# Performance work log

Measured on AMD Instinct MI355X. Metric: run time of the kernel, lower is better.

## Reference

```python
import jax, jax.numpy as jnp
import numpy as np

EPS = 1e-5

def _layer_norm(x, w, b):
    mu = jnp.mean(x, axis=-1, keepdims=True)
    var = jnp.mean((x - mu) ** 2, axis=-1, keepdims=True)
    return (x - mu) * jax.lax.rsqrt(var + EPS) * w + b

def setup_inputs() -> dict:
    H = 2048
    B, T = 4, 2048
    key = jax.random.key(0)
    ks = jax.random.split(key, 12)
    s = 0.02
    return {
        "hidden_state": jax.random.normal(ks[0], (B, T, H), dtype=jnp.float32),
        "ln_w": jnp.ones((H,), jnp.float32),
        "ln_b": jnp.zeros((H,), jnp.float32),
        "Wk": jax.random.normal(ks[1], (H, H), jnp.float32) * s,
        "Wv": jax.random.normal(ks[2], (H, H), jnp.float32) * s,
        "Wr": jax.random.normal(ks[3], (H, H), jnp.float32) * s,
        "Wo": jax.random.normal(ks[4], (H, H), jnp.float32) * s,
        "mix_k": jax.random.uniform(ks[5], (H,), jnp.float32),
        "mix_v": jax.random.uniform(ks[6], (H,), jnp.float32),
        "mix_r": jax.random.uniform(ks[7], (H,), jnp.float32),
        "time_decay": jax.random.normal(ks[8], (H,), jnp.float32) * 0.5,
        "current_token_weight": jax.random.normal(ks[9], (H,), jnp.float32) * 0.5,
    }

def _wkv(k, v, time_decay, curr_w):
    # k, v: [B, T, H]; max-stabilized RWKV recurrence, scanned over time.
    B, T, H = k.shape
    decay = -jnp.exp(time_decay)  # [H]
    num0 = jnp.zeros((B, H), k.dtype)
    den0 = jnp.zeros((B, H), k.dtype)
    norm0 = jnp.full((B, H), -jnp.inf, k.dtype)

    def step(carry, kv):
        num, den, norm = carry
        kt, vt = kv  # [B, H]
        ct = curr_w + kt
        cn = jnp.maximum(ct, norm)
        e_prev = jnp.exp(norm - cn)
        e_cur = jnp.exp(ct - cn)
        out = (e_prev * num + e_cur * vt) / (e_prev * den + e_cur)
        dpn = decay + norm
        new_norm = jnp.maximum(dpn, kt)
        e_d = jnp.exp(dpn - new_norm)
        e_k = jnp.exp(kt - new_norm)
        return (e_d * num + e_k * vt, e_d * den + e_k, new_norm), out

    kT = jnp.swapaxes(k, 0, 1)  # [T, B, H]
    vT = jnp.swapaxes(v, 0, 1)
    (num, den, norm), outs = jax.lax.scan(step, (num0, den0, norm0), (kT, vT))
    return jnp.swapaxes(outs, 0, 1), num, den, norm

def reference(hidden_state, ln_w, ln_b, Wk, Wv, Wr, Wo, mix_k, mix_v, mix_r,
              time_decay, current_token_weight):
    residual = hidden_state
    x = _layer_norm(hidden_state, ln_w, ln_b)  # [B, T, H]
    B, T, H = x.shape
    # shifted input: previous token (zeros for t=0 since previous_state is None)
    sx = jnp.concatenate([jnp.zeros((B, 1, H), x.dtype), x[:, :-1, :]], axis=1)
    xk = sx + mix_k * (x - sx)
    xv = sx + mix_v * (x - sx)
    xr = sx + mix_r * (x - sx)
    r = jax.nn.sigmoid(jnp.einsum('bth,oh->bto', xr, Wr))
    k = jnp.einsum('bth,oh->bto', xk, Wk)
    v = jnp.einsum('bth,oh->bto', xv, Wv)
    wkv, num, den, norm = _wkv(k, v, time_decay, current_token_weight)
    rwkv = jnp.einsum('bth,oh->bto', r * wkv, Wo)
    out = residual + rwkv
    return (out, (x[:, -1, :], num, den, norm))
```

## Files before the change

kernel.cpp:

```cpp
#include <hip/hip_runtime.h>
#include <hip/hip_bf16.h>
#include <stdint.h>

#define B_ 4
#define T_ 2048
#define H_ 2048
#define BT_ (B_ * T_)
#define BH_ (B_ * H_)
#define CH_ 32
#define CL_ (T_ / CH_)
#define NKT_ (H_ / 64)

typedef __bf16 bf16x8 __attribute__((ext_vector_type(8)));
typedef float f32x4 __attribute__((ext_vector_type(4)));

__device__ inline void async16(const void* g, void* l) {
  __builtin_amdgcn_global_load_lds(
      (__attribute__((address_space(1))) uint32_t*)(void*)(uintptr_t)g,
      (__attribute__((address_space(3))) uint32_t*)l,
      16, 0, 0);
}

__global__ __launch_bounds__(256) void cvt_bf16_kernel(
    const float* __restrict__ w0, const float* __restrict__ w1,
    const float* __restrict__ w2, const float* __restrict__ w3,
    __bf16* __restrict__ dst ) {
  const float* srcs[4] = {w0, w1, w2, w3};
  const float* src = srcs[blockIdx.y];
  __bf16* d = dst + (size_t)blockIdx.y * H_ * H_;
  int i = (blockIdx.x * 256 + threadIdx.x) * 8;
  const float4* s4 = (const float4*)(src + i);
  float4 a = s4[0], b = s4[1];
  bf16x8 o;
  o[0] = (__bf16)a.x; o[1] = (__bf16)a.y; o[2] = (__bf16)a.z; o[3] = (__bf16)a.w;
  o[4] = (__bf16)b.x; o[5] = (__bf16)b.y; o[6] = (__bf16)b.z; o[7] = (__bf16)b.w;
  *(bf16x8*)(d + i) = o;
}

__global__ __launch_bounds__(256) void ln_mix_kernel(
    const float* __restrict__ h, const float* __restrict__ lnw,
    const float* __restrict__ lnb, const float* __restrict__ mk,
    const float* __restrict__ mv, const float* __restrict__ mr,
    __bf16* __restrict__ xk, __bf16* __restrict__ xv, __bf16* __restrict__ xr,
    float* __restrict__ xlast) {
  const int row = blockIdx.x;
  const int t = row & (T_ - 1);
  const int tid = threadIdx.x;
  const bool hasprev = (t != 0);

  const float4* cr = (const float4*)(h + (size_t)row * H_);
  float4 c0 = cr[tid * 2 + 0], c1 = cr[tid * 2 + 1];
  float4 p0 = {0.f, 0.f, 0.f, 0.f}, p1 = {0.f, 0.f, 0.f, 0.f};
  if (hasprev) {
    const float4* pr = (const float4*)(h + (size_t)(row - 1) * H_);
    p0 = pr[tid * 2 + 0]; p1 = pr[tid * 2 + 1];
  }
  float4 red;
  red.x = c0.x + c0.y + c0.z + c0.w + c1.x + c1.y + c1.z + c1.w;
  red.y = c0.x * c0.x + c0.y * c0.y + c0.z * c0.z + c0.w * c0.w +
          c1.x * c1.x + c1.y * c1.y + c1.z * c1.z + c1.w * c1.w;
  red.z = p0.x + p0.y + p0.z + p0.w + p1.x + p1.y + p1.z + p1.w;
  red.w = p0.x * p0.x + p0.y * p0.y + p0.z * p0.z + p0.w * p0.w +
          p1.x * p1.x + p1.y * p1.y + p1.z * p1.z + p1.w * p1.w;
  #pragma unroll
  for (int off = 32; off; off >>= 1) {
    red.x += __shfl_down(red.x, off);
    red.y += __shfl_down(red.y, off);
    red.z += __shfl_down(red.z, off);
    red.w += __shfl_down(red.w, off);
  }
  __shared__ float4 rbuf_[4];
  const int lane = tid & 63, wid = tid >> 6;
  if (lane == 0) rbuf_[wid] = red;
  __syncthreads();
  float4 tot;
  tot.x = rbuf_[0].x + rbuf_[1].x + rbuf_[2].x + rbuf_[3].x;
  tot.y = rbuf_[0].y + rbuf_[1].y + rbuf_[2].y + rbuf_[3].y;
  tot.z = rbuf_[0].z + rbuf_[1].z + rbuf_[2].z + rbuf_[3].z;
  tot.w = rbuf_[0].w + rbuf_[1].w + rbuf_[2].w + rbuf_[3].w;

  const float inv = 1.0f / (float)H_;
  float mu = tot.x * inv;
  float rstd = rsqrtf(fmaxf(tot.y * inv - mu * mu, 0.f) + 1e-5f);
  float mup = tot.z * inv;
  float rstdp = rsqrtf(fmaxf(tot.w * inv - mup * mup, 0.f) + 1e-5f);

  float xc[8] = {c0.x, c0.y, c0.z, c0.w, c1.x, c1.y, c1.z, c1.w};
  float xp[8] = {p0.x, p0.y, p0.z, p0.w, p1.x, p1.y, p1.z, p1.w};
  const float4* W4 = (const float4*)lnw;
  const float4* Bv4 = (const float4*)lnb;
  const float4* MK4 = (const float4*)mk;
  const float4* MV4 = (const float4*)mv;
  const float4* MR4 = (const float4*)mr;
  float4 w0 = W4[tid * 2], w1 = W4[tid * 2 + 1];
  float4 b0 = Bv4[tid * 2], b1 = Bv4[tid * 2 + 1];
  float4 k0 = MK4[tid * 2], k1 = MK4[tid * 2 + 1];
  float4 v0 = MV4[tid * 2], v1 = MV4[tid * 2 + 1];
  float4 r0 = MR4[tid * 2], r1 = MR4[tid * 2 + 1];
  float wa[8] = {w0.x, w0.y, w0.z, w0.w, w1.x, w1.y, w1.z, w1.w};
  float ba[8] = {b0.x, b0.y, b0.z, b0.w, b1.x, b1.y, b1.z, b1.w};
  float ka[8] = {k0.x, k0.y, k0.z, k0.w, k1.x, k1.y, k1.z, k1.w};
  float va[8] = {v0.x, v0.y, v0.z, v0.w, v1.x, v1.y, v1.z, v1.w};
  float ra[8] = {r0.x, r0.y, r0.z, r0.w, r1.x, r1.y, r1.z, r1.w};

  bf16x8 ok_, ov_, or_;
  float xls[8];
  #pragma unroll
  for (int e = 0; e < 8; e++) {
    float x = (xc[e] - mu) * rstd * wa[e] + ba[e];
    float sx = hasprev ? (xp[e] - mup) * rstdp * wa[e] + ba[e] : 0.f;
    ok_[e] = (__bf16)(sx + ka[e] * (x - sx));
    ov_[e] = (__bf16)(sx + va[e] * (x - sx));
    or_[e] = (__bf16)(sx + ra[e] * (x - sx));
    xls[e] = x;
  }
  size_t obase = (size_t)row * H_ + tid * 8;
  *(bf16x8*)(xk + obase) = ok_;
  *(bf16x8*)(xv + obase) = ov_;
  *(bf16x8*)(xr + obase) = or_;
  if (t == T_ - 1) {
    float* dst = xlast + (size_t)(row >> 11) * H_ + tid * 8;
    #pragma unroll
    for (int e = 0; e < 8; e++) dst[e] = xls[e];
  }
}

template <int WO>
__global__ __launch_bounds__(256, 2) void gemm128(
    const __bf16* __restrict__ A0, const __bf16* __restrict__ A1,
    const __bf16* __restrict__ A2, const __bf16* __restrict__ Wb,
    __bf16* __restrict__ o0, __bf16* __restrict__ o1, __bf16* __restrict__ o2,
    float* __restrict__ outf, const float* __restrict__ resid) {
  __shared__ __align__(16) char ring[2][32768];

  const int NB = WO ? 1024 : 3072;
  const int wgid = blockIdx.x;
  const int lin = (wgid & 7) * (NB / 8) + (wgid >> 3);
  int z, l;
  if (WO) { z = 0; l = lin; }
  else    { z = lin >> 10; l = lin & 1023; }
  const int bm = l >> 4;
  const int bn = l & 15;

  const __bf16* A = (WO || z == 0) ? A0 : (z == 1 ? A1 : A2);
  const __bf16* Bw = Wb + (size_t)z * H_ * H_;
  __bf16* ob = (z == 0) ? o0 : (z == 1 ? o1 : o2);

  const int tid = threadIdx.x;
  const int lane = tid & 63, wv = tid >> 6;
  const int wm = wv >> 1;
  const int wn = wv & 1;
  const int rr = lane & 15, q = lane >> 4;

  f32x4 acc[4][4];
  #pragma unroll
  for (int m = 0; m < 4; m++)
    #pragma unroll
    for (int n = 0; n < 4; n++) acc[m][n] = (f32x4){0.f, 0.f, 0.f, 0.f};

  const char* Ag = (const char*)A + (size_t)(bm * 128) * (H_ * 2);
  const char* Bg = (const char*)Bw + (size_t)(bn * 128) * (H_ * 2);

  const int srow = wv * 8 + (lane >> 3);
  const int scol = ((lane & 7) ^ (lane >> 3)) << 4;
  const int rsw = rr & 7;

#define STAGE_TILE(kt_, buf_)                                                   \
  {                                                                             \
    char* base_ = ring[buf_];                                                   \
    _Pragma("unroll")                                                           \
    for (int mh_ = 0; mh_ < 2; mh_++) {                                         \
      const char* Mg_ = mh_ ? Bg : Ag;                                          \
      _Pragma("unroll")                                                         \
      for (int rd_ = 0; rd_ < 4; rd_++) {                                       \
        char* dst_ = base_ + mh_ * 16384 + rd_ * 4096 + wv * 1024;              \
        const char* src_ = Mg_ + (size_t)(rd_ * 32 + srow) * (H_ * 2)           \
                           + (kt_) * 128 + scol;                                \
        async16(src_, dst_);                                                    \
      }                                                                         \
    }                                                                           \
  }

  STAGE_TILE(0, 0);
  asm volatile("s_waitcnt vmcnt(0)" ::: "memory");
  __builtin_amdgcn_s_barrier();

  for (int kt = 0; kt < NKT_; kt++) {
    const int cur = kt & 1, nxt = cur ^ 1;
    const char* Alds = ring[cur];
    const char* Blds = ring[cur] + 16384;

    if (kt + 1 < NKT_) STAGE_TILE(kt + 1, nxt);

    bf16x8 bfr[4][2];
    #pragma unroll
    for (int ni = 0; ni < 4; ni++)
      #pragma unroll
      for (int ks = 0; ks < 2; ks++) {
        int row_t = wn * 64 + ni * 16 + rr;
        bfr[ni][ks] = *(const bf16x8*)(Blds + row_t * 128 +
                                       (((ks * 4 + q) ^ rsw) << 4));
      }

    #pragma unroll
    for (int mi = 0; mi < 4; mi++) {
      bf16x8 af[2];
      #pragma unroll
      for (int ks = 0; ks < 2; ks++) {
        int row_t = wm * 64 + mi * 16 + rr;
        af[ks] = *(const bf16x8*)(Alds + row_t * 128 +
                                  (((ks * 4 + q) ^ rsw) << 4));
      }
      #pragma unroll
      for (int ks = 0; ks < 2; ks++)
        #pragma unroll
        for (int ni = 0; ni < 4; ni++)
          acc[mi][ni] = __builtin_amdgcn_mfma_f32_16x16x32_bf16(
              af[ks], bfr[ni][ks], acc[mi][ni], 0, 0, 0);
    }

    if (kt + 1 < NKT_) {
      asm volatile("s_waitcnt vmcnt(0)" ::: "memory");
      __builtin_amdgcn_s_barrier();
    }
  }
#undef STAGE_TILE

  const int r0 = bm * 128 + wm * 64 + q * 4;
  const int c0 = bn * 128 + wn * 64 + rr;
  #pragma unroll
  for (int mi = 0; mi < 4; mi++) {
    #pragma unroll
    for (int ni = 0; ni < 4; ni++) {
      int col = c0 + ni * 16;
      #pragma unroll
      for (int rg = 0; rg < 4; rg++) {
        int rowg = r0 + mi * 16 + rg;
        size_t idx = (size_t)rowg * H_ + col;
        float vv = acc[mi][ni][rg];
        if (WO) {
          outf[idx] = resid[idx] + vv;
        } else if (z == 2) {
          ob[idx] = (__bf16)(1.f / (1.f + __expf(-vv)));
        } else {
          ob[idx] = (__bf16)vv;
        }
      }
    }
  }
}

__global__ __launch_bounds__(256) void wkv_pass1(
    const __bf16* __restrict__ k, const __bf16* __restrict__ v,
    const float* __restrict__ td,
    float* __restrict__ cs_num, float* __restrict__ cs_den,
    float* __restrict__ cs_norm) {
  const int id = blockIdx.x * 256 + threadIdx.x;
  const int c = blockIdx.y;
  const int b = id >> 11;
  const int hh = id & (H_ - 1);
  const float decay = -__expf(td[hh]);
  float num = 0.f, den = 0.f, norm = -INFINITY;

  const int UN = 16;
  for (int t0 = c * CL_; t0 < (c + 1) * CL_; t0 += UN) {
    float kk[UN], vv[UN];
    size_t base = ((size_t)b * T_ + t0) * H_ + hh;
    #pragma unroll
    for (int i = 0; i < UN; i++) {
      kk[i] = (float)k[base + (size_t)i * H_];
      vv[i] = (float)v[base + (size_t)i * H_];
    }
    #pragma unroll
    for (int i = 0; i < UN; i++) {
      float dpn = decay + norm;
      float nn = fmaxf(dpn, kk[i]);
      float ed = __expf(dpn - nn), ek = __expf(kk[i] - nn);
      num = ed * num + ek * vv[i];
      den = ed * den + ek;
      norm = nn;
    }
  }
  cs_num[c * BH_ + id] = num;
  cs_den[c * BH_ + id] = den;
  cs_norm[c * BH_ + id] = norm;
}

__global__ __launch_bounds__(256) void wkv_scan(
    const float* __restrict__ cs_num, const float* __restrict__ cs_den,
    const float* __restrict__ cs_norm, const float* __restrict__ td,
    float* __restrict__ px_num, float* __restrict__ px_den,
    float* __restrict__ px_norm) {
  const int id = blockIdx.x * 256 + threadIdx.x;
  const int hh = id & (H_ - 1);
  const float Lw = -__expf(td[hh]) * (float)CL_;
  float num = 0.f, den = 0.f, norm = -INFINITY;
  for (int c = 0; c < CH_; c++) {
    px_num[c * BH_ + id] = num;
    px_den[c * BH_ + id] = den;
    px_norm[c * BH_ + id] = norm;
    float n_c = cs_num[c * BH_ + id];
    float d_c = cs_den[c * BH_ + id];
    float m_c = cs_norm[c * BH_ + id];
    float sn = norm + Lw;
    float on = fmaxf(sn, m_c);
    float ea = __expf(sn - on), eb = __expf(m_c - on);
    num = ea * num + eb * n_c;
    den = ea * den + eb * d_c;
    norm = on;
  }
}

__global__ __launch_bounds__(256) void wkv_pass2(
    const __bf16* __restrict__ k, const __bf16* __restrict__ v,
    const __bf16* __restrict__ r, const float* __restrict__ td,
    const float* __restrict__ cw,
    const float* __restrict__ px_num, const float* __restrict__ px_den,
    const float* __restrict__ px_norm,
    __bf16* __restrict__ a, float* __restrict__ ndn) {
  const int id = blockIdx.x * 256 + threadIdx.x;
  const int c = blockIdx.y;
  const int b = id >> 11;
  const int hh = id & (H_ - 1);
  const float decay = -__expf(td[hh]);
  const float cwv = cw[hh];
  float num = px_num[c * BH_ + id];
  float den = px_den[c * BH_ + id];
  float norm = px_norm[c * BH_ + id];

  const int UN = 16;
  for (int t0 = c * CL_; t0 < (c + 1) * CL_; t0 += UN) {
    float kk[UN], vv[UN], rrv[UN];
    size_t base = ((size_t)b * T_ + t0) * H_ + hh;
    #pragma unroll
    for (int i = 0; i < UN; i++) {
      kk[i] = (float)k[base + (size_t)i * H_];
      vv[i] = (float)v[base + (size_t)i * H_];
      rrv[i] = (float)r[base + (size_t)i * H_];
    }
    #pragma unroll
    for (int i = 0; i < UN; i++) {
      float kt = kk[i], vt = vv[i];
      float ct = cwv + kt;
      float cn = fmaxf(ct, norm);
      float ep = __expf(norm - cn), ec = __expf(ct - cn);
      float o = (ep * num + ec * vt) / (ep * den + ec);
      a[base + (size_t)i * H_] = (__bf16)(rrv[i] * o);
      float dpn = decay + norm;
      float nn = fmaxf(dpn, kt);
      float ed = __expf(dpn - nn), ek = __expf(kt - nn);
      num = ed * num + ek * vt;
      den = ed * den + ek;
      norm = nn;
    }
  }
  if (c == CH_ - 1) {
    ndn[id] = num;
    ndn[BH_ + id] = den;
    ndn[2 * BH_ + id] = norm;
  }
}

extern "C" void kernel_launch(void* const* d_in, const int* in_sizes, int n_in,
                              void* d_out, int out_size, void* d_ws, size_t ws_size,
                              hipStream_t stream) {
  const float* h   = (const float*)d_in[0];
  const float* lnw = (const float*)d_in[1];
  const float* lnb = (const float*)d_in[2];
  const float* Wk  = (const float*)d_in[3];
  const float* Wv  = (const float*)d_in[4];
  const float* Wr  = (const float*)d_in[5];
  const float* Wo  = (const float*)d_in[6];
  const float* mk  = (const float*)d_in[7];
  const float* mv  = (const float*)d_in[8];
  const float* mr  = (const float*)d_in[9];
  const float* td  = (const float*)d_in[10];
  const float* cw  = (const float*)d_in[11];

  char* ws = (char*)d_ws;
  const size_t MB = 1048576;
  __bf16* xk   = (__bf16*)(ws);
  __bf16* xv   = (__bf16*)(ws + 32 * MB);
  __bf16* xr   = (__bf16*)(ws + 64 * MB);
  __bf16* kbuf = (__bf16*)(ws + 96 * MB);
  __bf16* vbuf = (__bf16*)(ws + 128 * MB);
  __bf16* W16  = (__bf16*)(ws + 160 * MB);
  __bf16* rbuf = (__bf16*)(ws + 192 * MB);
  __bf16* Wo16 = W16 + 3 * (size_t)H_ * H_;
  float* cs_num  = (float*)(ws + 64 * MB);
  float* cs_den  = cs_num + (size_t)CH_ * BH_;
  float* cs_norm = cs_den + (size_t)CH_ * BH_;
  float* px_num  = cs_norm + (size_t)CH_ * BH_;
  float* px_den  = px_num + (size_t)CH_ * BH_;
  float* px_norm = px_den + (size_t)CH_ * BH_;

  float* out  = (float*)d_out;
  float* xlast = out + (size_t)BT_ * H_;
  float* ndn   = xlast + (size_t)B_ * H_;

  dim3 cg((H_ * H_) / (256 * 8), 4);
  cvt_bf16_kernel<<<cg, 256, 0, stream>>>(Wk, Wv, Wr, Wo, W16);

  ln_mix_kernel<<<BT_, 256, 0, stream>>>(h, lnw, lnb, mk, mv, mr, xk, xv, xr, xlast);

  gemm128<0><<<3072, 256, 0, stream>>>(xk, xv, xr, W16, kbuf, vbuf, rbuf,
                                       nullptr, nullptr);

  dim3 wg(BH_ / 256, CH_);
  wkv_pass1<<<wg, 256, 0, stream>>>(kbuf, vbuf, td, cs_num, cs_den, cs_norm);
  wkv_scan<<<BH_ / 256, 256, 0, stream>>>(cs_num, cs_den, cs_norm, td,
                                          px_num, px_den, px_norm);
  wkv_pass2<<<wg, 256, 0, stream>>>(kbuf, vbuf, rbuf, td, cw,
                                    px_num, px_den, px_norm,
                                    xk , ndn);

  gemm128<1><<<1024, 256, 0, stream>>>(xk, nullptr, nullptr, Wo16,
                                       nullptr, nullptr, nullptr, out, h);
}
```

Before: 400.5 us.

## Split GEMM into dedicated KVR and Wo kernels with larger Wo tiles

Replaces the templated GEMM with two kernels. The fused K/V/R GEMM gets a new block-index swizzle that groups 8 M-tiles per N column for L2 reuse. The output projection becomes a 256x256-tile, 512-thread kernel with 128KB of double-buffered LDS, which raises arithmetic intensity per loaded tile. The trade-off is lower occupancy (one block per CU) and only 256 blocks for that GEMM, which may underfill the device.

```diff
diff --git a/kernel.cpp b/kernel.cpp
--- a/kernel.cpp
+++ b/kernel.cpp
@@ -125,24 +125,21 @@
   }
 }
 
-template <int WO>
-__global__ __launch_bounds__(256, 2) void gemm128(
+__global__ __launch_bounds__(256, 2) void gemm_kvr(
     const __bf16* __restrict__ A0, const __bf16* __restrict__ A1,
     const __bf16* __restrict__ A2, const __bf16* __restrict__ Wb,
-    __bf16* __restrict__ o0, __bf16* __restrict__ o1, __bf16* __restrict__ o2,
-    float* __restrict__ outf, const float* __restrict__ resid) {
+    __bf16* __restrict__ o0, __bf16* __restrict__ o1, __bf16* __restrict__ o2) {
   __shared__ __align__(16) char ring[2][32768];
 
-  const int NB = WO ? 1024 : 3072;
   const int wgid = blockIdx.x;
-  const int lin = (wgid & 7) * (NB / 8) + (wgid >> 3);
-  int z, l;
-  if (WO) { z = 0; l = lin; }
-  else    { z = lin >> 10; l = lin & 1023; }
-  const int bm = l >> 4;
-  const int bn = l & 15;
-
-  const __bf16* A = (WO || z == 0) ? A0 : (z == 1 ? A1 : A2);
+  const int z = wgid >> 10;
+  const int g = wgid & 1023;
+  const int x = g & 7;
+  const int i = g >> 3;
+  const int bm = x * 8 + (i & 7);
+  const int bn = i >> 3;
+
+  const __bf16* A = (z == 0) ? A0 : (z == 1 ? A1 : A2);
   const __bf16* Bw = Wb + (size_t)z * H_ * H_;
   __bf16* ob = (z == 0) ? o0 : (z == 1 ? o1 : o2);
 
@@ -238,13 +235,125 @@
         int rowg = r0 + mi * 16 + rg;
         size_t idx = (size_t)rowg * H_ + col;
         float vv = acc[mi][ni][rg];
-        if (WO) {
-          outf[idx] = resid[idx] + vv;
-        } else if (z == 2) {
+        if (z == 2) {
           ob[idx] = (__bf16)(1.f / (1.f + __expf(-vv)));
         } else {
           ob[idx] = (__bf16)vv;
         }
+      }
+    }
+  }
+}
+
+__global__ __launch_bounds__(512, 1) void gemm_wo(
+    const __bf16* __restrict__ A, const __bf16* __restrict__ Bw,
+    float* __restrict__ outf, const float* __restrict__ resid) {
+  __shared__ __align__(16) char ring[2][65536];
+
+  const int wgid = blockIdx.x;
+  const int lin = (wgid & 7) * 32 + (wgid >> 3);
+  const int bm = lin >> 3;
+  const int bn = lin & 7;
+
+  const int tid = threadIdx.x;
+  const int lane = tid & 63, wv = tid >> 6;
+  const int wm = wv >> 2;
+  const int wn = wv & 3;
+  const int rr = lane & 15, q = lane >> 4;
+
+  f32x4 acc[8][4];
+  #pragma unroll
+  for (int m = 0; m < 8; m++)
+    #pragma unroll
+    for (int n = 0; n < 4; n++) acc[m][n] = (f32x4){0.f, 0.f, 0.f, 0.f};
+
+  const char* Ag = (const char*)A + (size_t)(bm * 256) * (H_ * 2);
+  const char* Bg = (const char*)Bw + (size_t)(bn * 256) * (H_ * 2);
+
+  const int srow = wv * 8 + (lane >> 3);
+  const int scol = ((lane & 7) ^ (lane >> 3)) << 4;
+  const int rsw = rr & 7;
+
+#define STAGE_TILE(kt_, buf_)                                                   \
+  {                                                                             \
+    char* base_ = ring[buf_];                                                   \
+    _Pragma("unroll")                                                           \
+    for (int mh_ = 0; mh_ < 2; mh_++) {                                         \
+      const char* Mg_ = mh_ ? Bg : Ag;                                          \
+      _Pragma("unroll")                                                         \
+      for (int hh_ = 0; hh_ < 2; hh_++) {                                       \
+        _Pragma("unroll")                                                       \
+        for (int rd_ = 0; rd_ < 2; rd_++) {                                     \
+          char* dst_ = base_ + mh_ * 32768 + hh_ * 16384 + rd_ * 8192 + wv * 1024; \
+          const char* src_ = Mg_ + (size_t)(hh_ * 128 + rd_ * 64 + srow) * (H_ * 2) \
+                             + (kt_) * 128 + scol;                              \
+          async16(src_, dst_);                                                  \
+        }                                                                       \
+      }                                                                         \
+    }                                                                           \
+  }
+
+  STAGE_TILE(0, 0);
+  asm volatile("s_waitcnt vmcnt(0)" ::: "memory");
+  __builtin_amdgcn_s_barrier();
+
+  for (int kt = 0; kt < NKT_; kt++) {
+    const int cur = kt & 1, nxt = cur ^ 1;
+    const char* Alds = ring[cur];
+    const char* Blds = ring[cur] + 32768;
+
+    if (kt + 1 < NKT_) STAGE_TILE(kt + 1, nxt);
+
+    bf16x8 bfr[4][2];
+    #pragma unroll
+    for (int ni = 0; ni < 4; ni++)
+      #pragma unroll
+      for (int ks = 0; ks < 2; ks++) {
+        int row_t = wn * 64 + ni * 16 + rr;
+        bfr[ni][ks] = *(const bf16x8*)(Blds + row_t * 128 +
+                                       (((ks * 4 + q) ^ rsw) << 4));
+      }
+
+    #pragma unroll
+    for (int p = 0; p < 4; p++) {
+      bf16x8 af[2][2];
+      #pragma unroll
+      for (int mi = 0; mi < 2; mi++)
+        #pragma unroll
+        for (int ks = 0; ks < 2; ks++) {
+          int row_t = wm * 128 + p * 32 + mi * 16 + rr;
+          af[mi][ks] = *(const bf16x8*)(Alds + row_t * 128 +
+                                        (((ks * 4 + q) ^ rsw) << 4));
+        }
+      #pragma unroll
+      for (int ks = 0; ks < 2; ks++)
+        #pragma unroll
+        for (int mi = 0; mi < 2; mi++)
+          #pragma unroll
+          for (int ni = 0; ni < 4; ni++)
+            acc[p * 2 + mi][ni] = __builtin_amdgcn_mfma_f32_16x16x32_bf16(
+                af[mi][ks], bfr[ni][ks], acc[p * 2 + mi][ni], 0, 0, 0);
+    }
+
+    if (kt + 1 < NKT_) {
+      asm volatile("s_waitcnt vmcnt(0)" ::: "memory");
+      __builtin_amdgcn_s_barrier();
+    }
+  }
+#undef STAGE_TILE
+
+  const int r0 = bm * 256 + wm * 128 + q * 4;
+  const int c0 = bn * 256 + wn * 64 + rr;
+  #pragma unroll
+  for (int m = 0; m < 8; m++) {
+    #pragma unroll
+    for (int n = 0; n < 4; n++) {
+      int col = c0 + n * 16;
+      #pragma unroll
+      for (int rg = 0; rg < 4; rg++) {
+        int rowg = r0 + m * 16 + rg;
+        size_t idx = (size_t)rowg * H_ + col;
+        outf[idx] = resid[idx] + acc[m][n][rg];
       }
     }
   }
@@ -403,8 +512,7 @@
 
   ln_mix_kernel<<<BT_, 256, 0, stream>>>(h, lnw, lnb, mk, mv, mr, xk, xv, xr, xlast);
 
-  gemm128<0><<<3072, 256, 0, stream>>>(xk, xv, xr, W16, kbuf, vbuf, rbuf,
-                                       nullptr, nullptr);
+  gemm_kvr<<<3072, 256, 0, stream>>>(xk, xv, xr, W16, kbuf, vbuf, rbuf);
 
   dim3 wg(BH_ / 256, CH_);
   wkv_pass1<<<wg, 256, 0, stream>>>(kbuf, vbuf, td, cs_num, cs_den, cs_norm);
@@ -414,6 +522,5 @@
                                     px_num, px_den, px_norm,
                                     xk , ndn);
 
-  gemm128<1><<<1024, 256, 0, stream>>>(xk, nullptr, nullptr, Wo16,
-                                       nullptr, nullptr, nullptr, out, h);
-}
+  gemm_wo<<<256, 512, 0, stream>>>(xk, Wo16, out, h);
+}
```

After: 384.6 us. 1.04x faster.
